# Kernel optimization log

Hardware: AMD Instinct MI355X
Metric: run time of the kernel (lower is better)

The kernel has to match this reference:

```python
import jax, jax.numpy as jnp
import numpy as np

H_SPLITS = [2, 3, 3]          # crpe_window {3:2, 5:3, 7:3}
K_SIZES = [3, 5, 7]
NUM_HEADS = 8
EPS = 1e-6


def dwconv(x, w, b, k):
    # x: (B,C,H,W), w: (C,1,k,k) depthwise, 'same' padding
    y = jax.lax.conv_general_dilated(
        x, w, (1, 1), [(k // 2, k // 2)] * 2,
        feature_group_count=x.shape[1],
        dimension_numbers=('NCHW', 'OIHW', 'NCHW'))
    return y + b[None, :, None, None]


def layernorm(x, g, b):
    m = jnp.mean(x, -1, keepdims=True)
    v = jnp.var(x, -1, keepdims=True)
    return (x - m) * jax.lax.rsqrt(v + EPS) * g + b


def conv_rel_pos_enc(q, v, ws, bs, H, W):
    # ConvRelPosEnc (MPViT style, no cls token): q * depthwise_conv(v)
    B, h, N, Ch = q.shape
    v_img = v.transpose(0, 1, 3, 2).reshape(B, h * Ch, H, W)  # B (h Ch) H W
    splits = np.cumsum([hs * Ch for hs in H_SPLITS])[:-1]
    parts = jnp.split(v_img, splits, axis=1)
    conv_v = jnp.concatenate(
        [dwconv(p, w, b, k) for p, w, b, k in zip(parts, ws, bs, K_SIZES)], axis=1)
    conv_v = conv_v.reshape(B, h, Ch, N).transpose(0, 1, 3, 2)
    return q * conv_v


def setup_inputs() -> dict:
    key = jax.random.key(0)
    B, H, W, C, nd, r, mr = 8, 64, 64, 320, 4, 2, 4
    h = NUM_HEADS
    N = H * W
    Ch = C // h
    hid = C // r
    ks = jax.random.split(key, 16)
    s = 0.02
    return {
        'x': jax.random.normal(ks[0], (B, N, C), jnp.float32),
        'domain_label': jax.nn.one_hot(jax.random.randint(ks[1], (B,), 0, nd), nd, dtype=jnp.float32),
        'cpe_w': jax.random.normal(ks[2], (C, 1, 3, 3), jnp.float32) * s,
        'cpe_b': jnp.zeros((C,), jnp.float32),
        'ln1_g': jnp.ones((C,), jnp.float32), 'ln1_b': jnp.zeros((C,), jnp.float32),
        'qkv_w': jax.random.normal(ks[3], (3 * C, C), jnp.float32) * s,
        'qkv_b': jnp.zeros((3 * C,), jnp.float32),
        'crpe_w3': jax.random.normal(ks[4], (2 * Ch, 1, 3, 3), jnp.float32) * s,
        'crpe_b3': jnp.zeros((2 * Ch,), jnp.float32),
        'crpe_w5': jax.random.normal(ks[5], (3 * Ch, 1, 5, 5), jnp.float32) * s,
        'crpe_b5': jnp.zeros((3 * Ch,), jnp.float32),
        'crpe_w7': jax.random.normal(ks[6], (3 * Ch, 1, 7, 7), jnp.float32) * s,
        'crpe_b7': jnp.zeros((3 * Ch,), jnp.float32),
        'dom_w1': jax.random.normal(ks[7], (hid, nd), jnp.float32) * s,
        'dom_b1': jnp.zeros((hid,), jnp.float32),
        'dom_w2': jax.random.normal(ks[8], (C, hid), jnp.float32) * s,
        'dom_b2': jnp.zeros((C,), jnp.float32),
        'proj_w': jax.random.normal(ks[9], (C, C), jnp.float32) * s,
        'proj_b': jnp.zeros((C,), jnp.float32),
        'ln2_g': jnp.ones((C,), jnp.float32), 'ln2_b': jnp.zeros((C,), jnp.float32),
        'mlp_w1': jax.random.normal(ks[10], (mr * C, C), jnp.float32) * s,
        'mlp_b1': jnp.zeros((mr * C,), jnp.float32),
        'mlp_w2': jax.random.normal(ks[11], (C, mr * C), jnp.float32) * s,
        'mlp_b2': jnp.zeros((C,), jnp.float32),
        'H': H, 'W': W,
    }


def reference(x, domain_label, cpe_w, cpe_b, ln1_g, ln1_b, qkv_w, qkv_b,
              crpe_w3, crpe_b3, crpe_w5, crpe_b5, crpe_w7, crpe_b7,
              dom_w1, dom_b1, dom_w2, dom_b2, proj_w, proj_b,
              ln2_g, ln2_b, mlp_w1, mlp_b1, mlp_w2, mlp_b2, H, W):
    B, N, C = x.shape
    h = NUM_HEADS
    Ch = C // h
    scale = Ch ** -0.5
    # ConvPosEnc: depthwise 3x3 conv + residual
    img = x.transpose(0, 2, 1).reshape(B, C, H, W)
    x = (dwconv(img, cpe_w, cpe_b, 3) + img).reshape(B, C, N).transpose(0, 2, 1)
    # FactorAtt_ConvRelPosEnc_Sup
    cur = layernorm(x, ln1_g, ln1_b)
    qkv = (cur @ qkv_w.T + qkv_b).reshape(B, N, 3, h, Ch).transpose(2, 0, 3, 1, 4)
    q, k, v = qkv[0], qkv[1], qkv[2]          # (B,h,N,Ch) each
    k_sm = jax.nn.softmax(k, axis=2)          # softmax over tokens
    kv = jnp.einsum('bhnk,bhnv->bhkv', k_sm, v)   # (B,h,Ch,Ch)
    fa = jnp.einsum('bhnk,bhkv->bhnv', q, kv)
    fa = scale * fa + conv_rel_pos_enc(
        q, v, (crpe_w3, crpe_w5, crpe_w7), (crpe_b3, crpe_b5, crpe_b7), H, W)
    # domain gate: MLP(one_hot) -> softmax over heads, broadcast over tokens
    d = jax.nn.relu(domain_label @ dom_w1.T + dom_b1) @ dom_w2.T + dom_b2  # (B,C)
    d = jax.nn.softmax(d.reshape(B, h, 1, Ch), axis=1)
    att = (d * fa).transpose(0, 2, 1, 3).reshape(B, N, C)
    x = x + (att @ proj_w.T + proj_b)
    # MLP (GELU, ratio 4)
    cur = layernorm(x, ln2_g, ln2_b)
    cur = jax.nn.gelu(cur @ mlp_w1.T + mlp_b1, approximate=False) @ mlp_w2.T + mlp_b2
    return x + cur
```

## Files before the change

kernel.cpp:

```cpp
#include <hip/hip_runtime.h>
#include <hip/hip_bf16.h>
#include <math.h>
#include <type_traits>

#define B_    8
#define Nn    4096
#define Cc    320
#define QS    1024
#define ATT_SCALE 0.15811388300841897f

typedef __attribute__((ext_vector_type(8))) short s8v;
typedef __attribute__((ext_vector_type(4))) float f4v;

__device__ __forceinline__ float bf2f(short u) {
    return __uint_as_float(((unsigned int)(unsigned short)u) << 16);
}
__device__ __forceinline__ short f2bf(float f) {
    return (short)__bfloat16_as_ushort(__float2bfloat16(f));
}
__device__ __forceinline__ float gelu_fast(float v) {
    float u = v * (0.7978845608f + 0.0356774081f * v * v);
    float e = __expf(2.f * u);
    float t = 1.f - 2.f / (e + 1.f);
    return 0.5f * v * (1.f + t);
}

typedef const __attribute__((address_space(1))) unsigned int* gp1_t;
typedef __attribute__((address_space(3))) unsigned int* lp3_t;
__device__ __forceinline__ void gload16(const void* g, void* l) {
    __builtin_amdgcn_global_load_lds((gp1_t)g, (lp3_t)l, 16, 0, 0);
}

__global__ void cvt_all(const float* __restrict__ s0, const float* __restrict__ s1,
                        const float* __restrict__ s2, const float* __restrict__ s3,
                        __hip_bfloat16* __restrict__ d) {
    int i = blockIdx.x * 256 + threadIdx.x;
    if (i >= 1351680) return;
    const float* s; int j, rows, K;
    if (i < 327680)      { s = s0; j = i;          rows = 960;  K = 320; }
    else if (i < 450560) { s = s1; j = i - 327680; rows = 320;  K = 320; }
    else if (i < 860160) { s = s2; j = i - 450560; rows = 1280; K = 320; }
    else                 { s = s3; j = i - 860160; rows = 320;  K = 1280; }
    float v = (j / K < rows) ? s[j] : 0.f;
    d[i] = __float2bfloat16(v);
}

template<typename T>
__global__ void ln_kernel(const T* __restrict__ x, const float* __restrict__ g,
                          const float* __restrict__ bt, __hip_bfloat16* __restrict__ out) {
    int bn = blockIdx.x;
    int lane = threadIdx.x;
    const T* row = x + (size_t)bn * Cc;
    float v[5];
    float s = 0.f, s2 = 0.f;
    #pragma unroll
    for (int i = 0; i < 5; ++i) {
        if constexpr (std::is_same<T, float>::value) v[i] = row[lane + 64 * i];
        else v[i] = bf2f(((const short*)row)[lane + 64 * i]);
        s += v[i];
        s2 += v[i] * v[i];
    }
    #pragma unroll
    for (int off = 32; off > 0; off >>= 1) {
        s  += __shfl_down(s, off);
        s2 += __shfl_down(s2, off);
    }
    s  = __shfl(s, 0);
    s2 = __shfl(s2, 0);
    float mean = s * (1.f / 320.f);
    float var  = s2 * (1.f / 320.f) - mean * mean;
    float rstd = rsqrtf(var + 1e-6f);
    __hip_bfloat16* orow = out + (size_t)bn * Cc;
    #pragma unroll
    for (int i = 0; i < 5; ++i) {
        int c = lane + 64 * i;
        orow[c] = __float2bfloat16((v[i] - mean) * rstd * g[c] + bt[c]);
    }
}

template<int ACT, int RES, int WF32, int WBF16, int KT>
__global__ __launch_bounds__(512) void gemm_mfma(
        const __hip_bfloat16* __restrict__ A, const __hip_bfloat16* __restrict__ W,
        const float* __restrict__ bias, const void* __restrict__ resv,
        float* __restrict__ outf, __hip_bfloat16* __restrict__ outb,
        int NS, int Nreal, int gy) {
    __shared__ __align__(16) short As[256 * 64];
    __shared__ __align__(16) short Bs[128 * 64];
    int bid = blockIdx.x;
    int grp8 = gy << 3;
    int grp = bid / grp8, rem = bid % grp8;
    int m0 = ((grp << 3) + (rem & 7)) << 8;
    int n0 = (rem >> 3) << 7;
    int tid = threadIdx.x;
    int w = tid >> 6, lane = tid & 63;
    int wr = w >> 1, wc = w & 1;
    int lrow = lane & 15, lk = lane >> 4;
    f4v acc[4][4];
    #pragma unroll
    for (int i = 0; i < 4; ++i)
        #pragma unroll
        for (int j = 0; j < 4; ++j) acc[i][j] = (f4v){0.f, 0.f, 0.f, 0.f};

    int srow = (w << 3) + (lane >> 3);
    int slot = lane & 7;

    #pragma unroll
    for (int k0 = 0; k0 < KT; k0 += 64) {
        __syncthreads();
        #pragma unroll
        for (int i = 0; i < 4; ++i) {
            int row = i * 64 + srow;
            int sk = (slot ^ (row & 7)) << 3;
            gload16(&A[(size_t)(m0 + row) * KT + k0 + sk], &As[i * 4096 + w * 512]);
        }
        #pragma unroll
        for (int i = 0; i < 2; ++i) {
            int row = i * 64 + srow;
            int sk = (slot ^ (row & 7)) << 3;
            gload16(&W[(size_t)(n0 + row) * KT + k0 + sk], &Bs[i * 4096 + w * 512]);
        }
        __syncthreads();
        #pragma unroll
        for (int ks = 0; ks < 2; ++ks) {
            s8v af[4], bf[4];
            #pragma unroll
            for (int mi = 0; mi < 4; ++mi) {
                int row = wr * 64 + mi * 16 + lrow;
                int s = (ks * 4 + lk) ^ (row & 7);
                af[mi] = *reinterpret_cast<const s8v*>(&As[row * 64 + s * 8]);
            }
            #pragma unroll
            for (int ni = 0; ni < 4; ++ni) {
                int row = wc * 64 + ni * 16 + lrow;
                int s = (ks * 4 + lk) ^ (row & 7);
                bf[ni] = *reinterpret_cast<const s8v*>(&Bs[row * 64 + s * 8]);
            }
            #pragma unroll
            for (int mi = 0; mi < 4; ++mi)
                #pragma unroll
                for (int ni = 0; ni < 4; ++ni)
                    acc[mi][ni] = __builtin_amdgcn_mfma_f32_16x16x32_bf16(bf[ni], af[mi], acc[mi][ni], 0, 0, 0);
        }
    }
    #pragma unroll
    for (int mi = 0; mi < 4; ++mi) {
        int m = m0 + wr * 64 + mi * 16 + lrow;
        #pragma unroll
        for (int ni = 0; ni < 4; ++ni) {
            int n = n0 + wc * 64 + ni * 16 + (lk << 2);
            if (n >= Nreal) continue;
            f4v v4 = acc[mi][ni];
            float4 bv = *reinterpret_cast<const float4*>(&bias[n]);
            v4[0] += bv.x; v4[1] += bv.y; v4[2] += bv.z; v4[3] += bv.w;
            if (RES == 1) {
                const float* res = (const float*)resv;
                float4 rv = *reinterpret_cast<const float4*>(&res[(size_t)m * NS + n]);
                v4[0] += rv.x; v4[1] += rv.y; v4[2] += rv.z; v4[3] += rv.w;
            } else if (RES == 2) {
                const short* res = (const short*)resv;
                short4 rv = *reinterpret_cast<const short4*>(&res[(size_t)m * NS + n]);
                v4[0] += bf2f(rv.x); v4[1] += bf2f(rv.y);
                v4[2] += bf2f(rv.z); v4[3] += bf2f(rv.w);
            }
            if (ACT == 1) {
                #pragma unroll
                for (int r = 0; r < 4; ++r) v4[r] = gelu_fast(v4[r]);
            }
            if (WF32)
                *reinterpret_cast<float4*>(&outf[(size_t)m * NS + n]) =
                    make_float4(v4[0], v4[1], v4[2], v4[3]);
            if (WBF16) {
                ushort4 u;
                u.x = (unsigned short)f2bf(v4[0]);
                u.y = (unsigned short)f2bf(v4[1]);
                u.z = (unsigned short)f2bf(v4[2]);
                u.w = (unsigned short)f2bf(v4[3]);
                *reinterpret_cast<ushort4*>(&outb[(size_t)m * NS + n]) = u;
            }
        }
    }
}

template<int ACT, int RES, int WF32, int WBF16, int KT>
__global__ __launch_bounds__(512) void gemm_fulln(
        const __hip_bfloat16* __restrict__ A, const __hip_bfloat16* __restrict__ W,
        const float* __restrict__ bias, const void* __restrict__ resv,
        float* __restrict__ outf, __hip_bfloat16* __restrict__ outb,
        int NS) {
    __shared__ __align__(16) short As[64 * 64];
    __shared__ __align__(16) short Ws[320 * 64];
    int tid = threadIdx.x;
    int m0 = blockIdx.x << 6;
    int w = tid >> 6, lane = tid & 63;
    int wr = w >> 2, wc = w & 3;
    int lrow = lane & 15, lk = lane >> 4;
    f4v acc[2][5];
    #pragma unroll
    for (int i = 0; i < 2; ++i)
        #pragma unroll
        for (int j = 0; j < 5; ++j) acc[i][j] = (f4v){0.f, 0.f, 0.f, 0.f};

    int srow = tid >> 3;
    int slot = tid & 7;

    #pragma unroll
    for (int k0 = 0; k0 < KT; k0 += 64) {
        __syncthreads();
        {
            int sk = (slot ^ (srow & 7)) << 3;
            gload16(&A[(size_t)(m0 + srow) * KT + k0 + sk], &As[w * 512]);
        }
        #pragma unroll
        for (int i = 0; i < 5; ++i) {
            int row = i * 64 + srow;
            int sk = (slot ^ (row & 7)) << 3;
            gload16(&W[(size_t)row * KT + k0 + sk], &Ws[i * 4096 + w * 512]);
        }
        __syncthreads();
        #pragma unroll
        for (int ks = 0; ks < 2; ++ks) {
            s8v af[2], bf[5];
            #pragma unroll
            for (int mi = 0; mi < 2; ++mi) {
                int row = wr * 32 + mi * 16 + lrow;
                int s = (ks * 4 + lk) ^ (row & 7);
                af[mi] = *reinterpret_cast<const s8v*>(&As[row * 64 + s * 8]);
            }
            #pragma unroll
            for (int ni = 0; ni < 5; ++ni) {
                int row = wc * 80 + ni * 16 + lrow;
                int s = (ks * 4 + lk) ^ (row & 7);
                bf[ni] = *reinterpret_cast<const s8v*>(&Ws[row * 64 + s * 8]);
            }
            #pragma unroll
            for (int mi = 0; mi < 2; ++mi)
                #pragma unroll
                for (int ni = 0; ni < 5; ++ni)
                    acc[mi][ni] = __builtin_amdgcn_mfma_f32_16x16x32_bf16(bf[ni], af[mi], acc[mi][ni], 0, 0, 0);
        }
    }
    #pragma unroll
    for (int mi = 0; mi < 2; ++mi) {
        int m = m0 + wr * 32 + mi * 16 + lrow;
        #pragma unroll
        for (int ni = 0; ni < 5; ++ni) {
            int n = wc * 80 + ni * 16 + (lk << 2);
            f4v v4 = acc[mi][ni];
            float4 bv = *reinterpret_cast<const float4*>(&bias[n]);
            v4[0] += bv.x; v4[1] += bv.y; v4[2] += bv.z; v4[3] += bv.w;
            if (RES == 1) {
                const float* res = (const float*)resv;
                float4 rv = *reinterpret_cast<const float4*>(&res[(size_t)m * NS + n]);
                v4[0] += rv.x; v4[1] += rv.y; v4[2] += rv.z; v4[3] += rv.w;
            } else if (RES == 2) {
                const short* res = (const short*)resv;
                short4 rv = *reinterpret_cast<const short4*>(&res[(size_t)m * NS + n]);
                v4[0] += bf2f(rv.x); v4[1] += bf2f(rv.y);
                v4[2] += bf2f(rv.z); v4[3] += bf2f(rv.w);
            }
            if (ACT == 1) {
                #pragma unroll
                for (int r = 0; r < 4; ++r) v4[r] = gelu_fast(v4[r]);
            }
            if (WF32)
                *reinterpret_cast<float4*>(&outf[(size_t)m * NS + n]) =
                    make_float4(v4[0], v4[1], v4[2], v4[3]);
            if (WBF16) {
                ushort4 u;
                u.x = (unsigned short)f2bf(v4[0]);
                u.y = (unsigned short)f2bf(v4[1]);
                u.z = (unsigned short)f2bf(v4[2]);
                u.w = (unsigned short)f2bf(v4[3]);
                *reinterpret_cast<ushort4*>(&outb[(size_t)m * NS + n]) = u;
            }
        }
    }
}

template<int KSZ, int EPI, typename ST>
__global__ __launch_bounds__(256) void dwconv_tile(
        const ST* __restrict__ src, int sstride, int scoff,
        const float* __restrict__ wts, const float* __restrict__ bias, int cbase, int ngrp,
        const void* __restrict__ aux0v,
        const float* __restrict__ aux1,
        __hip_bfloat16* __restrict__ outb) {
    constexpr int P = KSZ / 2;
    constexpr int S = 16 + 2 * P;
    __shared__ float vt[S * S * 8];
    __shared__ float ws_[8 * KSZ * KSZ];
    int blk = blockIdx.x;
    int tile = blk & 15;
    int g  = (blk >> 4) % ngrp;
    int b  = (blk >> 4) / ngrp;
    int ty0 = (tile >> 2) << 4;
    int tx0 = (tile & 3) << 4;
    int c0 = cbase + g * 8;
    int tid = threadIdx.x;
    for (int e = tid; e < 8 * KSZ * KSZ; e += 256)
        ws_[e] = wts[g * 8 * KSZ * KSZ + e];
    const ST* sb = src + (size_t)b * Nn * sstride + scoff + c0;
    for (int e = tid; e < S * S; e += 256) {
        int hy = e / S, hx = e % S;
        int gy = ty0 - P + hy, gx = tx0 - P + hx;
        float px8[8];
        #pragma unroll
        for (int j = 0; j < 8; ++j) px8[j] = 0.f;
        if ((unsigned)gy < 64u && (unsigned)gx < 64u) {
            const ST* p = &sb[(size_t)((gy << 6) + gx) * sstride];
            if constexpr (std::is_same<ST, float>::value) {
                float4 lo = reinterpret_cast<const float4*>(p)[0];
                float4 hi = reinterpret_cast<const float4*>(p)[1];
                px8[0] = lo.x; px8[1] = lo.y; px8[2] = lo.z; px8[3] = lo.w;
                px8[4] = hi.x; px8[5] = hi.y; px8[6] = hi.z; px8[7] = hi.w;
            } else {
                s8v v8 = *reinterpret_cast<const s8v*>(p);
                #pragma unroll
                for (int j = 0; j < 8; ++j) px8[j] = bf2f(v8[j]);
            }
        }
        #pragma unroll
        for (int j = 0; j < 8; ++j) vt[e * 8 + j] = px8[j];
    }
    __syncthreads();
    int cl  = tid & 7;
    int px  = (tid >> 3) & 15;
    int pyh = tid >> 7;
    int c = c0 + cl;
    float acc[8];
    float bval = bias[g * 8 + cl];
    #pragma unroll
    for (int j = 0; j < 8; ++j) acc[j] = bval;
    #pragma unroll
    for (int dx = 0; dx < KSZ; ++dx) {
        float col[8 + KSZ - 1];
        #pragma unroll
        for (int i = 0; i < 8 + KSZ - 1; ++i)
            col[i] = vt[((pyh * 8 + i) * S + (px + dx)) * 8 + cl];
        #pragma unroll
        for (int j = 0; j < 8; ++j)
            #pragma unroll
            for (int dy = 0; dy < KSZ; ++dy)
                acc[j] += col[j + dy] * ws_[cl * KSZ * KSZ + dy * KSZ + dx];
    }
    #pragma unroll
    for (int j = 0; j < 8; ++j) {
        int n = ((ty0 + pyh * 8 + j) << 6) + tx0 + px;
        size_t bn = (size_t)b * Nn + n;
        if (EPI == 0) {
            float ctr = vt[((pyh * 8 + j + P) * S + (px + P)) * 8 + cl];
            outb[bn * Cc + c] = __float2bfloat16(acc[j] + ctr);
        } else {
            const short* fa0 = (const short*)aux0v;
            float qv  = bf2f(((const short*)src)[bn * (size_t)sstride + c]);
            float fav = bf2f(fa0[bn * Cc + c]);
            float r = aux1[(size_t)b * Cc + c] * (ATT_SCALE * fav + qv * acc[j]);
            outb[bn * Cc + c] = __float2bfloat16(r);
        }
    }
}

__global__ __launch_bounds__(256) void kv_mfma(const __hip_bfloat16* __restrict__ qkv,
                                               float* __restrict__ kvp) {
    __shared__ short lds[4 * 2 * 48 * 66];
    int blk = blockIdx.x;
    int s = blk & 7;
    int bh = blk >> 3;
    int h = bh & 7, b = bh >> 3;
    int tid = threadIdx.x;
    int w = tid >> 6, lane = tid & 63;
    short* ke_t = lds + w * 2 * 48 * 66;
    short* vv_t = ke_t + 48 * 66;
    for (int e = lane; e < 8 * 66; e += 64) {
        ke_t[40 * 66 + e] = 0;
        vv_t[40 * 66 + e] = 0;
    }
    for (int n = lane; n < 66; n += 64) vv_t[40 * 66 + n] = (short)0x3F80;

    const short* kb = (const short*)qkv + (size_t)b * Nn * QS + 320 + h * 40;
    const short* vb = kb + 320;
    int col0 = lane & 15, kq = lane >> 4;
    f4v acc[3][3];
    #pragma unroll
    for (int i = 0; i < 3; ++i)
        #pragma unroll
        for (int j = 0; j < 3; ++j) acc[i][j] = (f4v){0.f, 0.f, 0.f, 0.f};

    for (int t = w; t < 8; t += 4) {
        int n0 = s * 512 + t * 64;
        for (int e = lane; e < 320; e += 64) {
            int nl = e / 5, oct = e % 5;
            size_t go = (size_t)(n0 + nl) * QS + oct * 8;
            s8v k8 = *reinterpret_cast<const s8v*>(kb + go);
            s8v v8 = *reinterpret_cast<const s8v*>(vb + go);
            #pragma unroll
            for (int j = 0; j < 8; ++j) {
                ke_t[(oct * 8 + j) * 66 + nl] = f2bf(__expf(bf2f(k8[j])));
                vv_t[(oct * 8 + j) * 66 + nl] = v8[j];
            }
        }
        __syncthreads();
        #pragma unroll
        for (int ks = 0; ks < 2; ++ks) {
            s8v af[3], bfr[3];
            #pragma unroll
            for (int mt = 0; mt < 3; ++mt)
                af[mt] = *reinterpret_cast<const s8v*>(ke_t + (mt * 16 + col0) * 66 + ks * 32 + kq * 8);
            #pragma unroll
            for (int nt = 0; nt < 3; ++nt)
                bfr[nt] = *reinterpret_cast<const s8v*>(vv_t + (nt * 16 + col0) * 66 + ks * 32 + kq * 8);
            #pragma unroll
            for (int mt = 0; mt < 3; ++mt)
                #pragma unroll
                for (int nt = 0; nt < 3; ++nt)
                    acc[mt][nt] = __builtin_amdgcn_mfma_f32_16x16x32_bf16(af[mt], bfr[nt], acc[mt][nt], 0, 0, 0);
        }
        __syncthreads();
    }
    float* red = (float*)lds;
    #pragma unroll
    for (int mt = 0; mt < 3; ++mt) {
        #pragma unroll
        for (int nt = 0; nt < 3; ++nt) {
            #pragma unroll
            for (int r = 0; r < 4; ++r) {
                int ch = mt * 16 + kq * 4 + r;
                int cv = nt * 16 + col0;
                if (ch < 40) red[w * 1920 + ch * 48 + cv] = acc[mt][nt][r];
            }
        }
    }
    __syncthreads();
    for (int p = tid; p < 1920; p += 256) {
        float sv = red[p] + red[1920 + p] + red[2 * 1920 + p] + red[3 * 1920 + p];
        kvp[(size_t)blk * 1920 + p] = sv;
    }
}

__global__ void kv_combine2(const float* __restrict__ kvp, float* __restrict__ kv) {
    int bh = blockIdx.x;
    int tid = threadIdx.x;
    __shared__ float sinv[40];
    if (tid < 40) {
        float S = 0.f;
        for (int s2 = 0; s2 < 8; ++s2)
            S += kvp[(size_t)(bh * 8 + s2) * 1920 + tid * 48 + 40];
        sinv[tid] = 1.f / S;
    }
    __syncthreads();
    for (int p = tid; p < 1600; p += 256) {
        int ch = p / 40, cv = p % 40;
        float v = 0.f;
        for (int s2 = 0; s2 < 8; ++s2)
            v += kvp[(size_t)(bh * 8 + s2) * 1920 + ch * 48 + cv];
        kv[(size_t)bh * 1600 + p] = v * sinv[ch];
    }
}

__global__ void dgate_kernel(const float* __restrict__ lbl, const float* __restrict__ w1,
                             const float* __restrict__ b1, const float* __restrict__ w2,
                             const float* __restrict__ b2, float* __restrict__ dg) {
    int b = blockIdx.x;
    int tid = threadIdx.x;
    __shared__ float hid[160];
    __shared__ float dd[320];
    if (tid < 160) {
        float a = b1[tid];
        for (int d = 0; d < 4; ++d) a += w1[tid * 4 + d] * lbl[b * 4 + d];
        hid[tid] = fmaxf(a, 0.f);
    }
    __syncthreads();
    float a = b2[tid];
    for (int j = 0; j < 160; ++j) a += w2[tid * 160 + j] * hid[j];
    dd[tid] = a;
    __syncthreads();
    if (tid < 40) {
        float M = -1e30f;
        for (int h2 = 0; h2 < 8; ++h2) M = fmaxf(M, dd[h2 * 40 + tid]);
        float S = 0.f;
        float e[8];
        for (int h2 = 0; h2 < 8; ++h2) { e[h2] = __expf(dd[h2 * 40 + tid] - M); S += e[h2]; }
        float inv = 1.f / S;
        for (int h2 = 0; h2 < 8; ++h2) dg[b * 320 + h2 * 40 + tid] = e[h2] * inv;
    }
}

__global__ __launch_bounds__(256) void fa_kernel(const __hip_bfloat16* __restrict__ qkv,
        const float* __restrict__ kvmat, __hip_bfloat16* __restrict__ fa) {
    __shared__ float kvs[1600];
    int blk = blockIdx.x;
    int chunk = blk & 15;
    int bh = blk >> 4;
    int h = bh & 7, b = bh >> 3;
    int tid = threadIdx.x;
    for (int e = tid; e < 1600; e += 256) kvs[e] = kvmat[(size_t)bh * 1600 + e];
    __syncthreads();
    int n = chunk * 256 + tid;
    const short* qr = (const short*)qkv + (size_t)(b * Nn + n) * QS + h * 40;
    float q[40];
    #pragma unroll
    for (int i = 0; i < 5; ++i) {
        s8v v8 = reinterpret_cast<const s8v*>(qr)[i];
        #pragma unroll
        for (int j = 0; j < 8; ++j) q[i * 8 + j] = bf2f(v8[j]);
    }
    float o[40];
    #pragma unroll
    for (int cv = 0; cv < 40; ++cv) o[cv] = 0.f;
    #pragma unroll
    for (int ch = 0; ch < 40; ++ch) {
        float qv = q[ch];
        #pragma unroll
        for (int cv = 0; cv < 40; ++cv)
            o[cv] += qv * kvs[ch * 40 + cv];
    }
    short* fr = (short*)fa + (size_t)(b * Nn + n) * 320 + h * 40;
    #pragma unroll
    for (int i = 0; i < 5; ++i) {
        s8v u;
        #pragma unroll
        for (int j = 0; j < 8; ++j) u[j] = f2bf(o[i * 8 + j]);
        *reinterpret_cast<s8v*>(fr + i * 8) = u;
    }
}

extern "C" void kernel_launch(void* const* d_in, const int* in_sizes, int n_in,
                              void* d_out, int out_size, void* d_ws, size_t ws_size,
                              hipStream_t stream) {
    const float* x     = (const float*)d_in[0];
    const float* lbl   = (const float*)d_in[1];
    const float* cpe_w = (const float*)d_in[2];
    const float* cpe_b = (const float*)d_in[3];
    const float* ln1g  = (const float*)d_in[4];
    const float* ln1b  = (const float*)d_in[5];
    const float* qkv_w = (const float*)d_in[6];
    const float* qkv_b = (const float*)d_in[7];
    const float* w3    = (const float*)d_in[8];
    const float* b3    = (const float*)d_in[9];
    const float* w5    = (const float*)d_in[10];
    const float* b5    = (const float*)d_in[11];
    const float* w7    = (const float*)d_in[12];
    const float* b7    = (const float*)d_in[13];
    const float* dw1   = (const float*)d_in[14];
    const float* db1   = (const float*)d_in[15];
    const float* dw2   = (const float*)d_in[16];
    const float* db2   = (const float*)d_in[17];
    const float* pw    = (const float*)d_in[18];
    const float* pb    = (const float*)d_in[19];
    const float* ln2g  = (const float*)d_in[20];
    const float* ln2b  = (const float*)d_in[21];
    const float* m1w   = (const float*)d_in[22];
    const float* m1b   = (const float*)d_in[23];
    const float* m2w   = (const float*)d_in[24];
    const float* m2b   = (const float*)d_in[25];
    float* out = (float*)d_out;

    float* ws = (float*)d_ws;
    __hip_bfloat16* x1b  = (__hip_bfloat16*)ws; ws += 5242880;
    __hip_bfloat16* qkvb = (__hip_bfloat16*)ws; ws += 16777216;
    float* big  = ws; ws += 20971520;
    __hip_bfloat16* gelub = (__hip_bfloat16*)big;
    __hip_bfloat16* fab   = (__hip_bfloat16*)ws; ws += 5242880;
    __hip_bfloat16* bb1   = (__hip_bfloat16*)ws; ws += 5242880;
    __hip_bfloat16* wb    = (__hip_bfloat16*)ws; ws += 675840;
    float* kvp  = ws; ws += 983040;
    float* kv   = ws; ws += 102400;
    float* dg   = ws; ws += 2560;
    __hip_bfloat16* wbq  = wb;
    __hip_bfloat16* wbp  = wbq  + 1024 * 320;
    __hip_bfloat16* wbm1 = wbp  + 384 * 320;
    __hip_bfloat16* wbm2 = wbm1 + 1280 * 320;

    cvt_all<<<5280, 256, 0, stream>>>(qkv_w, pw, m1w, m2w, wb);
    dwconv_tile<3, 0, float><<<B_ * 40 * 16, 256, 0, stream>>>(
        x, 320, 0, cpe_w, cpe_b, 0, 40, nullptr, nullptr, x1b);
    ln_kernel<__hip_bfloat16><<<B_ * Nn, 64, 0, stream>>>(x1b, ln1g, ln1b, bb1);
    gemm_mfma<0, 0, 0, 1, 320><<<1024, 512, 0, stream>>>(bb1, wbq, qkv_b, nullptr,
                                                         nullptr, qkvb, QS, 960, 8);
    kv_mfma<<<512, 256, 0, stream>>>(qkvb, kvp);
    kv_combine2<<<64, 256, 0, stream>>>(kvp, kv);
    dgate_kernel<<<B_, 320, 0, stream>>>(lbl, dw1, db1, dw2, db2, dg);
    fa_kernel<<<B_ * 8 * 16, 256, 0, stream>>>(qkvb, kv, fab);
    dwconv_tile<3, 1, __hip_bfloat16><<<B_ * 10 * 16, 256, 0, stream>>>(
        qkvb, QS, 640, w3, b3, 0, 10, fab, dg, bb1);
    dwconv_tile<5, 1, __hip_bfloat16><<<B_ * 15 * 16, 256, 0, stream>>>(
        qkvb, QS, 640, w5, b5, 80, 15, fab, dg, bb1);
    dwconv_tile<7, 1, __hip_bfloat16><<<B_ * 15 * 16, 256, 0, stream>>>(
        qkvb, QS, 640, w7, b7, 200, 15, fab, dg, bb1);
    gemm_fulln<0, 2, 1, 0, 320><<<512, 512, 0, stream>>>(bb1, wbp, pb, x1b,
                                                         out, nullptr, 320);
    ln_kernel<float><<<B_ * Nn, 64, 0, stream>>>(out, ln2g, ln2b, bb1);
    gemm_mfma<1, 0, 0, 1, 320><<<1280, 512, 0, stream>>>(bb1, wbm1, m1b, nullptr,
                                                         nullptr, gelub, 1280, 1280, 10);
    gemm_fulln<0, 1, 1, 0, 1280><<<512, 512, 0, stream>>>(gelub, wbm2, m2b, out,
                                                          out, nullptr, 320);
}
```

Measured before the change: 310.0 us.

## Fuse LayerNorm2 into proj GEMM epilogue and merge CRPE convs into one kernel

Each proj GEMM block covers all 320 columns of its 64 rows, so the epilogue now reduces row sums and squared sums through shared memory and writes the LayerNorm2 bf16 output directly. This removes the separate ln_kernel launch and its re-read of the fp32 residual. The three CRPE depthwise conv launches (3x3, 5x5, 7x7) become a single kernel that branches on channel group, which cuts launch overhead and lets all groups share one grid. In exchange, the one-pass variance formula is less numerically stable, and the merged kernel sizes its shared memory for the 7x7 case, which may lower occupancy for the smaller kernels.

```diff
diff --git a/kernel.cpp b/kernel.cpp
--- a/kernel.cpp
+++ b/kernel.cpp
@@ -181,12 +181,13 @@
     }
 }
 
-template<int ACT, int RES, int WF32, int WBF16, int KT>
+template<int ACT, int RES, int WF32, int WBF16, int KT, int LN>
 __global__ __launch_bounds__(512) void gemm_fulln(
         const __hip_bfloat16* __restrict__ A, const __hip_bfloat16* __restrict__ W,
         const float* __restrict__ bias, const void* __restrict__ resv,
-        float* __restrict__ outf, __hip_bfloat16* __restrict__ outb,
-        int NS) {
+        float* __restrict__ outf, __hip_bfloat16* __restrict__ outb, int NS,
+        const float* __restrict__ lng, const float* __restrict__ lnb,
+        __hip_bfloat16* __restrict__ lnout) {
     __shared__ __align__(16) short As[64 * 64];
     __shared__ __align__(16) short Ws[320 * 64];
     int tid = threadIdx.x;
@@ -239,6 +240,7 @@
                     acc[mi][ni] = __builtin_amdgcn_mfma_f32_16x16x32_bf16(bf[ni], af[mi], acc[mi][ni], 0, 0, 0);
         }
     }
+    float psum[2] = {0.f, 0.f}, psq[2] = {0.f, 0.f};
     #pragma unroll
     for (int mi = 0; mi < 2; ++mi) {
         int m = m0 + wr * 32 + mi * 16 + lrow;
@@ -273,32 +275,75 @@
                 u.w = (unsigned short)f2bf(v4[3]);
                 *reinterpret_cast<ushort4*>(&outb[(size_t)m * NS + n]) = u;
             }
-        }
-    }
-}
-
-template<int KSZ, int EPI, typename ST>
-__global__ __launch_bounds__(256) void dwconv_tile(
-        const ST* __restrict__ src, int sstride, int scoff,
-        const float* __restrict__ wts, const float* __restrict__ bias, int cbase, int ngrp,
-        const void* __restrict__ aux0v,
-        const float* __restrict__ aux1,
-        __hip_bfloat16* __restrict__ outb) {
-    constexpr int P = KSZ / 2;
-    constexpr int S = 16 + 2 * P;
+            if (LN) {
+                acc[mi][ni] = v4;
+                psum[mi] += v4[0] + v4[1] + v4[2] + v4[3];
+                psq[mi]  += v4[0]*v4[0] + v4[1]*v4[1] + v4[2]*v4[2] + v4[3]*v4[3];
+            }
+        }
+    }
+    if (LN) {
+        __syncthreads();
+        float* red = (float*)As;
+        #pragma unroll
+        for (int mi = 0; mi < 2; ++mi) {
+            int rl = wr * 32 + mi * 16 + lrow;
+            red[(rl * 16 + wc * 4 + lk) * 2]     = psum[mi];
+            red[(rl * 16 + wc * 4 + lk) * 2 + 1] = psq[mi];
+        }
+        __syncthreads();
+        float* st = (float*)Ws;
+        if (tid < 64) {
+            float s = 0.f, q = 0.f;
+            #pragma unroll
+            for (int p = 0; p < 16; ++p) {
+                s += red[(tid * 16 + p) * 2];
+                q += red[(tid * 16 + p) * 2 + 1];
+            }
+            float mean = s * (1.f / 320.f);
+            float var  = q * (1.f / 320.f) - mean * mean;
+            st[tid * 2]     = mean;
+            st[tid * 2 + 1] = rsqrtf(var + 1e-6f);
+        }
+        __syncthreads();
+        #pragma unroll
+        for (int mi = 0; mi < 2; ++mi) {
+            int rl = wr * 32 + mi * 16 + lrow;
+            int m = m0 + rl;
+            float mean = st[rl * 2], rstd = st[rl * 2 + 1];
+            #pragma unroll
+            for (int ni = 0; ni < 5; ++ni) {
+                int n = wc * 80 + ni * 16 + (lk << 2);
+                float4 g4 = *reinterpret_cast<const float4*>(&lng[n]);
+                float4 b4 = *reinterpret_cast<const float4*>(&lnb[n]);
+                f4v v4 = acc[mi][ni];
+                ushort4 u;
+                u.x = (unsigned short)f2bf((v4[0] - mean) * rstd * g4.x + b4.x);
+                u.y = (unsigned short)f2bf((v4[1] - mean) * rstd * g4.y + b4.y);
+                u.z = (unsigned short)f2bf((v4[2] - mean) * rstd * g4.z + b4.z);
+                u.w = (unsigned short)f2bf((v4[3] - mean) * rstd * g4.w + b4.w);
+                *reinterpret_cast<ushort4*>(&lnout[(size_t)m * Cc + n]) = u;
+            }
+        }
+    }
+}
+
+__global__ __launch_bounds__(256) void cpe_tile(
+        const float* __restrict__ src, const float* __restrict__ wts,
+        const float* __restrict__ bias, __hip_bfloat16* __restrict__ outb) {
+    constexpr int P = 1, S = 18;
     __shared__ float vt[S * S * 8];
-    __shared__ float ws_[8 * KSZ * KSZ];
+    __shared__ float ws_[8 * 9];
     int blk = blockIdx.x;
     int tile = blk & 15;
-    int g  = (blk >> 4) % ngrp;
-    int b  = (blk >> 4) / ngrp;
+    int g  = (blk >> 4) % 40;
+    int b  = (blk >> 4) / 40;
     int ty0 = (tile >> 2) << 4;
     int tx0 = (tile & 3) << 4;
-    int c0 = cbase + g * 8;
+    int c0 = g * 8;
     int tid = threadIdx.x;
-    for (int e = tid; e < 8 * KSZ * KSZ; e += 256)
-        ws_[e] = wts[g * 8 * KSZ * KSZ + e];
-    const ST* sb = src + (size_t)b * Nn * sstride + scoff + c0;
+    for (int e = tid; e < 72; e += 256) ws_[e] = wts[c0 * 9 + e];
+    const float* sb = src + (size_t)b * Nn * Cc + c0;
     for (int e = tid; e < S * S; e += 256) {
         int hy = e / S, hx = e % S;
         int gy = ty0 - P + hy, gx = tx0 - P + hx;
@@ -306,17 +351,11 @@
         #pragma unroll
         for (int j = 0; j < 8; ++j) px8[j] = 0.f;
         if ((unsigned)gy < 64u && (unsigned)gx < 64u) {
-            const ST* p = &sb[(size_t)((gy << 6) + gx) * sstride];
-            if constexpr (std::is_same<ST, float>::value) {
-                float4 lo = reinterpret_cast<const float4*>(p)[0];
-                float4 hi = reinterpret_cast<const float4*>(p)[1];
-                px8[0] = lo.x; px8[1] = lo.y; px8[2] = lo.z; px8[3] = lo.w;
-                px8[4] = hi.x; px8[5] = hi.y; px8[6] = hi.z; px8[7] = hi.w;
-            } else {
-                s8v v8 = *reinterpret_cast<const s8v*>(p);
-                #pragma unroll
-                for (int j = 0; j < 8; ++j) px8[j] = bf2f(v8[j]);
-            }
+            const float* p = &sb[(size_t)((gy << 6) + gx) * Cc];
+            float4 lo = reinterpret_cast<const float4*>(p)[0];
+            float4 hi = reinterpret_cast<const float4*>(p)[1];
+            px8[0] = lo.x; px8[1] = lo.y; px8[2] = lo.z; px8[3] = lo.w;
+            px8[4] = hi.x; px8[5] = hi.y; px8[6] = hi.z; px8[7] = hi.w;
         }
         #pragma unroll
         for (int j = 0; j < 8; ++j) vt[e * 8 + j] = px8[j];
@@ -327,36 +366,114 @@
     int pyh = tid >> 7;
     int c = c0 + cl;
     float acc[8];
-    float bval = bias[g * 8 + cl];
+    float bval = bias[c];
     #pragma unroll
     for (int j = 0; j < 8; ++j) acc[j] = bval;
     #pragma unroll
-    for (int dx = 0; dx < KSZ; ++dx) {
-        float col[8 + KSZ - 1];
-        #pragma unroll
-        for (int i = 0; i < 8 + KSZ - 1; ++i)
+    for (int dx = 0; dx < 3; ++dx) {
+        float col[10];
+        #pragma unroll
+        for (int i = 0; i < 10; ++i)
             col[i] = vt[((pyh * 8 + i) * S + (px + dx)) * 8 + cl];
         #pragma unroll
         for (int j = 0; j < 8; ++j)
             #pragma unroll
-            for (int dy = 0; dy < KSZ; ++dy)
-                acc[j] += col[j + dy] * ws_[cl * KSZ * KSZ + dy * KSZ + dx];
+            for (int dy = 0; dy < 3; ++dy)
+                acc[j] += col[j + dy] * ws_[cl * 9 + dy * 3 + dx];
     }
     #pragma unroll
     for (int j = 0; j < 8; ++j) {
         int n = ((ty0 + pyh * 8 + j) << 6) + tx0 + px;
         size_t bn = (size_t)b * Nn + n;
-        if (EPI == 0) {
-            float ctr = vt[((pyh * 8 + j + P) * S + (px + P)) * 8 + cl];
-            outb[bn * Cc + c] = __float2bfloat16(acc[j] + ctr);
-        } else {
-            const short* fa0 = (const short*)aux0v;
-            float qv  = bf2f(((const short*)src)[bn * (size_t)sstride + c]);
-            float fav = bf2f(fa0[bn * Cc + c]);
-            float r = aux1[(size_t)b * Cc + c] * (ATT_SCALE * fav + qv * acc[j]);
-            outb[bn * Cc + c] = __float2bfloat16(r);
-        }
-    }
+        float ctr = vt[((pyh * 8 + j + P) * S + (px + P)) * 8 + cl];
+        outb[bn * Cc + c] = __float2bfloat16(acc[j] + ctr);
+    }
+}
+
+template<int KSZ>
+__device__ __forceinline__ void crpe_body(
+        float* vt, float* ws_, int tile, int b, int c0,
+        const short* __restrict__ qkv, const float* __restrict__ wts,
+        const float* __restrict__ bias,
+        const short* __restrict__ fa0, const float* __restrict__ dg,
+        short* __restrict__ outb) {
+    constexpr int P = KSZ / 2;
+    constexpr int S = 16 + 2 * P;
+    int ty0 = (tile >> 2) << 4;
+    int tx0 = (tile & 3) << 4;
+    int tid = threadIdx.x;
+    for (int e = tid; e < 8 * KSZ * KSZ; e += 256) ws_[e] = wts[e];
+    const short* sb = qkv + (size_t)b * Nn * QS + 640 + c0;
+    for (int e = tid; e < S * S; e += 256) {
+        int hy = e / S, hx = e % S;
+        int gy = ty0 - P + hy, gx = tx0 - P + hx;
+        float px8[8];
+        #pragma unroll
+        for (int j = 0; j < 8; ++j) px8[j] = 0.f;
+        if ((unsigned)gy < 64u && (unsigned)gx < 64u) {
+            s8v v8 = *reinterpret_cast<const s8v*>(&sb[(size_t)((gy << 6) + gx) * QS]);
+            #pragma unroll
+            for (int j = 0; j < 8; ++j) px8[j] = bf2f(v8[j]);
+        }
+        #pragma unroll
+        for (int j = 0; j < 8; ++j) vt[e * 8 + j] = px8[j];
+    }
+    __syncthreads();
+    int cl  = tid & 7;
+    int px  = (tid >> 3) & 15;
+    int pyh = tid >> 7;
+    int c = c0 + cl;
+    float acc[8];
+    float bval = bias[cl];
+    #pragma unroll
+    for (int j = 0; j < 8; ++j) acc[j] = bval;
+    #pragma unroll
+    for (int dx = 0; dx < KSZ; ++dx) {
+        float col[8 + KSZ - 1];
+        #pragma unroll
+        for (int i = 0; i < 8 + KSZ - 1; ++i)
+            col[i] = vt[((pyh * 8 + i) * S + (px + dx)) * 8 + cl];
+        #pragma unroll
+        for (int j = 0; j < 8; ++j)
+            #pragma unroll
+            for (int dy = 0; dy < KSZ; ++dy)
+                acc[j] += col[j + dy] * ws_[cl * KSZ * KSZ + dy * KSZ + dx];
+    }
+    float dgv = dg[(size_t)b * Cc + c];
+    #pragma unroll
+    for (int j = 0; j < 8; ++j) {
+        int n = ((ty0 + pyh * 8 + j) << 6) + tx0 + px;
+        size_t bn = (size_t)b * Nn + n;
+        float qv  = bf2f(qkv[bn * QS + c]);
+        float fav = bf2f(fa0[bn * Cc + c]);
+        float r = dgv * (ATT_SCALE * fav + qv * acc[j]);
+        outb[bn * Cc + c] = __float2bfloat16(r);
+    }
+}
+
+__global__ __launch_bounds__(256) void crpe_all(
+        const __hip_bfloat16* __restrict__ qkv,
+        const float* __restrict__ w3, const float* __restrict__ b3,
+        const float* __restrict__ w5, const float* __restrict__ b5,
+        const float* __restrict__ w7, const float* __restrict__ b7,
+        const __hip_bfloat16* __restrict__ fa, const float* __restrict__ dg,
+        __hip_bfloat16* __restrict__ outb) {
+    __shared__ float vt[22 * 22 * 8];
+    __shared__ float ws_[8 * 49];
+    int blk = blockIdx.x;
+    int tile = blk & 15;
+    int g = (blk >> 4) % 40;
+    int b = (blk >> 4) / 40;
+    int c0 = g * 8;
+    if (g < 10)
+        crpe_body<3>(vt, ws_, tile, b, c0, (const short*)qkv,
+                     w3 + c0 * 9, b3 + c0, (const short*)fa, dg, (short*)outb);
+    else if (g < 25)
+        crpe_body<5>(vt, ws_, tile, b, c0, (const short*)qkv,
+                     w5 + (c0 - 80) * 25, b5 + (c0 - 80), (const short*)fa, dg, (short*)outb);
+    else
+        crpe_body<7>(vt, ws_, tile, b, c0, (const short*)qkv,
+                     w7 + (c0 - 200) * 49, b7 + (c0 - 200), (const short*)fa, dg, (short*)outb);
 }
 
 __global__ __launch_bounds__(256) void kv_mfma(const __hip_bfloat16* __restrict__ qkv,
@@ -571,8 +688,7 @@
     __hip_bfloat16* wbm2 = wbm1 + 1280 * 320;
 
     cvt_all<<<5280, 256, 0, stream>>>(qkv_w, pw, m1w, m2w, wb);
-    dwconv_tile<3, 0, float><<<B_ * 40 * 16, 256, 0, stream>>>(
-        x, 320, 0, cpe_w, cpe_b, 0, 40, nullptr, nullptr, x1b);
+    cpe_tile<<<B_ * 40 * 16, 256, 0, stream>>>(x, cpe_w, cpe_b, x1b);
     ln_kernel<__hip_bfloat16><<<B_ * Nn, 64, 0, stream>>>(x1b, ln1g, ln1b, bb1);
     gemm_mfma<0, 0, 0, 1, 320><<<1024, 512, 0, stream>>>(bb1, wbq, qkv_b, nullptr,
                                                          nullptr, qkvb, QS, 960, 8);
@@ -580,17 +696,14 @@
     kv_combine2<<<64, 256, 0, stream>>>(kvp, kv);
     dgate_kernel<<<B_, 320, 0, stream>>>(lbl, dw1, db1, dw2, db2, dg);
     fa_kernel<<<B_ * 8 * 16, 256, 0, stream>>>(qkvb, kv, fab);
-    dwconv_tile<3, 1, __hip_bfloat16><<<B_ * 10 * 16, 256, 0, stream>>>(
-        qkvb, QS, 640, w3, b3, 0, 10, fab, dg, bb1);
-    dwconv_tile<5, 1, __hip_bfloat16><<<B_ * 15 * 16, 256, 0, stream>>>(
-        qkvb, QS, 640, w5, b5, 80, 15, fab, dg, bb1);
-    dwconv_tile<7, 1, __hip_bfloat16><<<B_ * 15 * 16, 256, 0, stream>>>(
-        qkvb, QS, 640, w7, b7, 200, 15, fab, dg, bb1);
-    gemm_fulln<0, 2, 1, 0, 320><<<512, 512, 0, stream>>>(bb1, wbp, pb, x1b,
-                                                         out, nullptr, 320);
-    ln_kernel<float><<<B_ * Nn, 64, 0, stream>>>(out, ln2g, ln2b, bb1);
+    crpe_all<<<B_ * 40 * 16, 256, 0, stream>>>(qkvb, w3, b3, w5, b5, w7, b7,
+                                               fab, dg, bb1);
+    gemm_fulln<0, 2, 1, 0, 320, 1><<<512, 512, 0, stream>>>(bb1, wbp, pb, x1b,
+                                                            out, nullptr, 320,
+                                                            ln2g, ln2b, bb1);
     gemm_mfma<1, 0, 0, 1, 320><<<1280, 512, 0, stream>>>(bb1, wbm1, m1b, nullptr,
                                                          nullptr, gelub, 1280, 1280, 10);
-    gemm_fulln<0, 1, 1, 0, 1280><<<512, 512, 0, stream>>>(gelub, wbm2, m2b, out,
-                                                          out, nullptr, 320);
-}
+    gemm_fulln<0, 1, 1, 0, 1280, 0><<<512, 512, 0, stream>>>(gelub, wbm2, m2b, out,
+                                                             out, nullptr, 320,
+                                                             nullptr, nullptr, nullptr);
+}
```

Result: faster. 299.7 us (-3.3%).
